# Performance work log

Measured on AMD Instinct MI355X. Metric: run time of the kernel, lower is better.

The kernel has to match this reference:

```python
import jax, jax.numpy as jnp
import numpy as np

B, T, H, I = 256, 512, 512, 256  # max batch, seq_len, hidden_size, input_size


def setup_inputs() -> dict:
    key = jax.random.key(0)
    ks = jax.random.split(key, 8)
    rnn_input_data = jax.random.normal(ks[0], (B * T, I), jnp.float32)
    # descending packed batch sizes, first one = B (enforce_sorted semantics)
    bs = jnp.sort(jax.random.randint(ks[1], (T,), B // 2, B + 1))[::-1]
    batch_sizes = bs.at[0].set(B).astype(jnp.int32)
    h0 = 0.1 * jax.random.normal(ks[2], (1, B, H), jnp.float32)
    c0 = 0.1 * jax.random.normal(ks[3], (1, B, H), jnp.float32)
    W_w = jax.random.normal(ks[4], (I, 4 * H), jnp.float32) / np.sqrt(I).astype(np.float32)
    W_b = jnp.zeros((4 * H,), jnp.float32)
    U_w = jax.random.normal(ks[5], (H, 4 * H), jnp.float32) / np.sqrt(H).astype(np.float32)
    tau = jnp.asarray(0.02, jnp.float32)
    return {"rnn_input_data": rnn_input_data, "batch_sizes": batch_sizes,
            "h0": h0, "c0": c0, "tau": tau, "W_w": W_w, "W_b": W_b, "U_w": U_w}


def reference(rnn_input_data, batch_sizes, h0, c0, tau, W_w, W_b, U_w):
    L, Bm, Hd = h0.shape
    SD = 2  # state_dim, fixed by the 2x2 A matrix
    mhu = 1.5
    A = jnp.array([[mhu, -mhu], [1.0 / mhu, 0.0]], jnp.float32)
    # faithful to source bug: data is always sliced from the front -> only first B rows used
    x0 = rnn_input_data[:Bm]  # (B, I), masked per step
    Tn = batch_sizes.shape[0]
    arangeB = jnp.arange(Bm)

    def step(carry, inp):
        h, c = carry  # (L,B,H) each
        t, bs = inp
        mask = (arangeB < bs)[:, None]  # (B,1)
        # tau-based state-space correction on first SD dims of ALL layers/rows (t != 0)
        xs = h[:, :, :SD]
        xcorr = xs + tau * jnp.einsum('lbi,ij->lbj', xs, A)
        h = h.at[:, :, :SD].set(jnp.where(t != 0, xcorr, xs))
        # single LSTMCell (num_layers == 1)
        gates = x0 @ W_w + W_b + h[0] @ U_w  # (B, 4H)
        i, f, g, o = jnp.split(gates, 4, axis=-1)
        c_new = jax.nn.sigmoid(f) * c[0] + jax.nn.sigmoid(i) * jnp.tanh(g)
        h_new = jax.nn.sigmoid(o) * jnp.tanh(c_new)
        h = h.at[0].set(jnp.where(mask, h_new, h[0]))
        c = c.at[0].set(jnp.where(mask, c_new, c[0]))
        out_t = jnp.where(mask, h[-1], 0.0)  # outputs[t, :bs] = h[-1,:bs], rest zeros
        return (h, c), out_t

    (h, c), outputs = jax.lax.scan(step, (h0, c0), (jnp.arange(Tn), batch_sizes))
    return outputs, h, c
```

## Files before the change

### kernel.cpp

```cpp
#include <hip/hip_runtime.h>


#define TN 512
#define BM 256
#define HD 512
#define ID 256

typedef __attribute__((ext_vector_type(8))) __bf16 bf16x8;
typedef __attribute__((ext_vector_type(4))) __bf16 bf16x4;
typedef __attribute__((ext_vector_type(4))) unsigned int u32x4;
typedef __attribute__((ext_vector_type(4))) float f32x4;

union ABits { u32x4 u; bf16x8 b; };
union U64x1 { bf16x4 v; unsigned long long q; };

__device__ __forceinline__ float sigm(float x) { return 1.f / (1.f + __expf(-x)); }
__device__ __forceinline__ float tanh_fast(float x) { return 1.f - 2.f / (__expf(2.f * x) + 1.f); }

__device__ __forceinline__ void store_h64(__bf16* p, unsigned long long v) {
    asm volatile("global_store_dwordx2 %0, %1, off sc0" :: "v"(p), "v"(v) : "memory");
}

__global__ void __launch_bounds__(256, 1)
lstm_persist(const float* __restrict__ x_in, const int* __restrict__ bs_in,
             const float* __restrict__ h0, const float* __restrict__ c0,
             const float* __restrict__ tau_p, const float* __restrict__ Ww,
             const float* __restrict__ Wb, const float* __restrict__ Uw,
             float* __restrict__ out, __bf16* __restrict__ hbuf,
             int* __restrict__ flags)
{
    __shared__ int   bs_lds[TN];
    __shared__ float x0_lds[16][ID + 1];
    __shared__ float hn_patch[4][16][9];
    __shared__ __align__(16) __bf16 htile[16][520];

    const int tid  = threadIdx.x;
    const int lane = tid & 63;
    const int w    = tid >> 6;
    const int bid  = blockIdx.x;

    const int xcd = bid & 7;
    const int ii  = bid >> 3;
    const int mg  = xcd * 2 + (ii >> 4);
    const int jb  = ii & 15;

    const int row0 = mg * 16;
    const int j0   = jb * 32;
    const int l15  = lane & 15;
    const int kg   = lane >> 4;
    const int gq   = lane & 3;
    const int jjq  = l15 >> 2;
    const float tau = tau_p[0];

    const int srow = 4 * w + (lane >> 4);
    const int scol = (lane & 15) * 8;

    for (int i = tid; i < TN; i += 256) bs_lds[i] = bs_in[i];
    for (int s = tid; s < 16 * (ID / 4); s += 256) {
        int r = s >> 6, cs = s & 63;
        *reinterpret_cast<float4*>(&x0_lds[r][cs * 4]) =
            reinterpret_cast<const float4*>(x_in + (size_t)(row0 + r) * ID)[cs];
    }
    __syncthreads();

    float gxv[2][4];
    {
        float a[2][4] = {};
        const int cbase = j0 + 8 * w + kg;
        for (int k = 0; k < ID; ++k) {
            float xv = x0_lds[l15][k];
            const float* wr = Ww + (size_t)k * 2048;
            #pragma unroll
            for (int g = 0; g < 4; ++g) {
                a[0][g] += xv * wr[g * HD + cbase];
                a[1][g] += xv * wr[g * HD + cbase + 4];
            }
        }
        #pragma unroll
        for (int g = 0; g < 4; ++g) {
            gxv[0][g] = a[0][g] + Wb[g * HD + cbase];
            gxv[1][g] = a[1][g] + Wb[g * HD + cbase + 4];
        }
    }

    bf16x8 ub[2][16];
    #pragma unroll
    for (int f = 0; f < 2; ++f) {
        const int ucol = gq * HD + j0 + 8 * w + 4 * f + jjq;
        #pragma unroll
        for (int ki = 0; ki < 16; ++ki) {
            const int kb = ki * 32 + kg * 8;
            bf16x8 v;
            #pragma unroll
            for (int e = 0; e < 8; ++e) v[e] = (__bf16)Uw[(size_t)(kb + e) * 2048 + ucol];
            ub[f][ki] = v;
        }
    }

    float creg[2];
    #pragma unroll
    for (int f = 0; f < 2; ++f)
        creg[f] = c0[(size_t)(row0 + l15) * HD + j0 + 8 * w + 4 * f + kg];

    const int sr = lane >> 1, ss = lane & 1;
    const int jc = j0 + 8 * w + 4 * ss;
    const bool is_store = (lane < 32);
    const bool owner = (jb == 0) && (w == 0) && (ss == 0) && is_store;
    float hprev[4] = {0.f, 0.f, 0.f, 0.f};
    float hxy0 = 0.f, hxy1 = 0.f;

    if (is_store) {
        float4 v = *reinterpret_cast<const float4*>(h0 + (size_t)(row0 + sr) * HD + jc);
        hprev[0] = v.x; hprev[1] = v.y; hprev[2] = v.z; hprev[3] = v.w;
        if (owner) { hxy0 = v.x; hxy1 = v.y; }
        U64x1 sv;
        #pragma unroll
        for (int c = 0; c < 4; ++c) sv.v[c] = (__bf16)hprev[c];
        store_h64(hbuf + (size_t)(row0 + sr) * HD + jc, sv.q);
    }
    asm volatile("s_waitcnt vmcnt(0)" ::: "memory");
    __builtin_amdgcn_sched_barrier(0);
    if (lane == 0)
        __hip_atomic_store(&flags[mg * 64 + jb * 4 + w], 1,
                           __ATOMIC_RELAXED, __HIP_MEMORY_SCOPE_AGENT);

    for (int t = 0; t < TN; ++t) {
        const __bf16* base_p = hbuf + (size_t)(t & 1) * (BM * HD);
        __bf16*       base_n = hbuf + (size_t)((t + 1) & 1) * (BM * HD);
        const int bs_t = bs_lds[t];

        if (t != 0) {
            float xs0 = hxy0, xs1 = hxy1;
            hxy0 = xs0 + tau * (1.5f * xs0 + 0.66666667f * xs1);
            hxy1 = xs1 + tau * (-1.5f * xs0);
        }

        for (int it = 0; it < (1 << 20); ++it) {
            int v = __hip_atomic_load(&flags[mg * 64 + lane],
                                      __ATOMIC_RELAXED, __HIP_MEMORY_SCOPE_AGENT);
            if (__all(v >= t + 1)) break;
            __builtin_amdgcn_s_sleep(1);
        }

        {
            const __bf16* srcp = base_p + (size_t)(row0 + srow) * HD + scol;
            u32x4 s0, s1, s2, s3;
            asm volatile(
                "global_load_dwordx4 %0, %[p], off sc0\n\t"
                "global_load_dwordx4 %1, %[p], off offset:256 sc0\n\t"
                "global_load_dwordx4 %2, %[p], off offset:512 sc0\n\t"
                "global_load_dwordx4 %3, %[p], off offset:768 sc0\n\t"
                "s_waitcnt vmcnt(0)"
                : "=&v"(s0), "=&v"(s1), "=&v"(s2), "=&v"(s3)
                : [p] "v"(srcp)
                : "memory");
            __builtin_amdgcn_sched_barrier(0);
            ABits tb;
            tb.u = s0; *reinterpret_cast<bf16x8*>(&htile[srow][scol])       = tb.b;
            tb.u = s1; *reinterpret_cast<bf16x8*>(&htile[srow][scol + 128]) = tb.b;
            tb.u = s2; *reinterpret_cast<bf16x8*>(&htile[srow][scol + 256]) = tb.b;
            tb.u = s3; *reinterpret_cast<bf16x8*>(&htile[srow][scol + 384]) = tb.b;
        }
        __syncthreads();

        bf16x8 ah[16];
        #pragma unroll
        for (int ki = 0; ki < 16; ++ki)
            ah[ki] = *reinterpret_cast<const bf16x8*>(&htile[l15][ki * 32 + kg * 8]);

        if (t != 0 && kg == 0) {
            float xs0 = (float)ah[0][0];
            float xs1 = (float)ah[0][1];
            ah[0][0] = (__bf16)(xs0 + tau * (1.5f * xs0 + 0.66666667f * xs1));
            ah[0][1] = (__bf16)(xs1 + tau * (-1.5f * xs0));
        }

        f32x4 acc0 = {0.f, 0.f, 0.f, 0.f}, acc1 = {0.f, 0.f, 0.f, 0.f};
        #pragma unroll
        for (int ki = 0; ki < 16; ++ki) {
            acc0 = __builtin_amdgcn_mfma_f32_16x16x32_bf16(ub[0][ki], ah[ki], acc0, 0, 0, 0);
            acc1 = __builtin_amdgcn_mfma_f32_16x16x32_bf16(ub[1][ki], ah[ki], acc1, 0, 0, 0);
        }

        const bool act_m = (row0 + l15) < bs_t;
        #pragma unroll
        for (int f = 0; f < 2; ++f) {
            const f32x4 a = f ? acc1 : acc0;
            float gi = a[0] + gxv[f][0];
            float gf = a[1] + gxv[f][1];
            float gg = a[2] + gxv[f][2];
            float go = a[3] + gxv[f][3];
            float cn = sigm(gf) * creg[f] + sigm(gi) * tanh_fast(gg);
            float hn = sigm(go) * tanh_fast(cn);
            if (act_m) creg[f] = cn;
            hn_patch[w][l15][4 * f + kg] = hn;
        }

        asm volatile("s_waitcnt lgkmcnt(0)" ::: "memory");
        __builtin_amdgcn_sched_barrier(0);

        if (is_store) {
            const bool act_r = (row0 + sr) < bs_t;
            float hn0 = hn_patch[w][sr][4 * ss + 0];
            float hn1 = hn_patch[w][sr][4 * ss + 1];
            float hn2 = hn_patch[w][sr][4 * ss + 2];
            float hn3 = hn_patch[w][sr][4 * ss + 3];
            float hv[4];
            hv[0] = act_r ? hn0 : hprev[0];
            hv[1] = act_r ? hn1 : hprev[1];
            hv[2] = act_r ? hn2 : hprev[2];
            hv[3] = act_r ? hn3 : hprev[3];
            if (owner) {
                if (act_r) { hxy0 = hn0; hxy1 = hn1; }
                else       { hv[0] = hxy0; hv[1] = hxy1; }
            }
            #pragma unroll
            for (int c = 0; c < 4; ++c) hprev[c] = hv[c];
            U64x1 sv;
            #pragma unroll
            for (int c = 0; c < 4; ++c) sv.v[c] = (__bf16)hv[c];
            store_h64(base_n + (size_t)(row0 + sr) * HD + jc, sv.q);
            asm volatile("s_waitcnt vmcnt(0)" ::: "memory");
            __builtin_amdgcn_sched_barrier(0);
            if (lane == 0)
                __hip_atomic_store(&flags[mg * 64 + jb * 4 + w], t + 2,
                                   __ATOMIC_RELAXED, __HIP_MEMORY_SCOPE_AGENT);
            float4 q;
            q.x = act_r ? hn0 : 0.f; q.y = act_r ? hn1 : 0.f;
            q.z = act_r ? hn2 : 0.f; q.w = act_r ? hn3 : 0.f;
            *reinterpret_cast<float4*>(out + (size_t)t * (BM * HD)
                                       + (size_t)(row0 + sr) * HD + jc) = q;
        }
    }

    if (is_store) {
        float4 p;
        p.x = hprev[0]; p.y = hprev[1]; p.z = hprev[2]; p.w = hprev[3];
        *reinterpret_cast<float4*>(out + (size_t)TN * BM * HD
                                   + (size_t)(row0 + sr) * HD + jc) = p;
    }
    {
        float* cp = out + (size_t)TN * BM * HD + (size_t)BM * HD;
        #pragma unroll
        for (int f = 0; f < 2; ++f)
            cp[(size_t)(row0 + l15) * HD + j0 + 8 * w + 4 * f + kg] = creg[f];
    }
}

extern "C" void kernel_launch(void* const* d_in, const int* in_sizes, int n_in,
                              void* d_out, int out_size, void* d_ws, size_t ws_size,
                              hipStream_t stream) {
    const float* x_in = (const float*)d_in[0];
    const int*   bs   = (const int*)d_in[1];
    const float* h0   = (const float*)d_in[2];
    const float* c0   = (const float*)d_in[3];
    const float* tau  = (const float*)d_in[4];
    const float* Ww   = (const float*)d_in[5];
    const float* Wb   = (const float*)d_in[6];
    const float* Uw   = (const float*)d_in[7];
    float* out = (float*)d_out;

    int*    flags = (int*)d_ws;
    __bf16* hbuf  = (__bf16*)((char*)d_ws + 4096);

    (void)hipMemsetAsync(d_ws, 0, 4096, stream);

    hipLaunchKernelGGL(lstm_persist, dim3(256), dim3(256), 0, stream,
                       x_in, bs, h0, c0, tau, Ww, Wb, Uw, out, hbuf, flags);
}
```

Measured before the change: 2.366 ms.

## Load h operands straight into registers, drop LDS staging and skip inactive row groups

Each wave now loads its own 16 rows of the previous hidden state directly from global memory into MFMA operand registers. This removes the LDS tile, the block-wide __syncthreads, and the LDS round-trip used to transpose the gate outputs, which are now redistributed with cross-lane shuffles. Row groups entirely beyond the current batch size skip the wait, the GEMM and the flag update and only write zeros. The trade-off is four times more global load traffic per wave (redundant across waves) and a skip path that relies on descending batch sizes so consumers never wait on the skipped flags.

After: 3.682 ms. 55.6% more time.

```diff
diff --git a/kernel.cpp b/kernel.cpp
--- a/kernel.cpp
+++ b/kernel.cpp
@@ -31,8 +31,6 @@
 {
     __shared__ int   bs_lds[TN];
     __shared__ float x0_lds[16][ID + 1];
-    __shared__ float hn_patch[4][16][9];
-    __shared__ __align__(16) __bf16 htile[16][520];
 
     const int tid  = threadIdx.x;
     const int lane = tid & 63;
@@ -52,9 +50,6 @@
     const int jjq  = l15 >> 2;
     const float tau = tau_p[0];
 
-    const int srow = 4 * w + (lane >> 4);
-    const int scol = (lane & 15) * 8;
-
     for (int i = tid; i < TN; i += 256) bs_lds[i] = bs_in[i];
     for (int s = tid; s < 16 * (ID / 4); s += 256) {
         int r = s >> 6, cs = s & 63;
@@ -102,8 +97,9 @@
     for (int f = 0; f < 2; ++f)
         creg[f] = c0[(size_t)(row0 + l15) * HD + j0 + 8 * w + 4 * f + kg];
 
-    const int sr = lane >> 1, ss = lane & 1;
-    const int jc = j0 + 8 * w + 4 * ss;
+    const int sr   = lane >> 1, ss = lane & 1;
+    const int sr16 = (lane >> 1) & 15;
+    const int jc   = j0 + 8 * w + 4 * ss;
     const bool is_store = (lane < 32);
     const bool owner = (jb == 0) && (w == 0) && (ss == 0) && is_store;
     float hprev[4] = {0.f, 0.f, 0.f, 0.f};
@@ -135,6 +131,15 @@
             hxy1 = xs1 + tau * (-1.5f * xs0);
         }
 
+        if (row0 >= bs_t) {
+            if (is_store) {
+                float4 z = {0.f, 0.f, 0.f, 0.f};
+                *reinterpret_cast<float4*>(out + (size_t)t * (BM * HD)
+                                           + (size_t)(row0 + sr) * HD + jc) = z;
+            }
+            continue;
+        }
+
         for (int it = 0; it < (1 << 20); ++it) {
             int v = __hip_atomic_load(&flags[mg * 64 + lane],
                                       __ATOMIC_RELAXED, __HIP_MEMORY_SCOPE_AGENT);
@@ -142,31 +147,46 @@
             __builtin_amdgcn_s_sleep(1);
         }
 
+        const __bf16* arow = base_p + (size_t)(row0 + l15) * HD + kg * 8;
+        u32x4 r0,r1,r2,r3,r4,r5,r6,r7,r8,r9,r10,r11,r12,r13,r14,r15;
+        asm volatile(
+            "global_load_dwordx4 %0, %[p], off sc0\n\t"
+            "global_load_dwordx4 %1, %[p], off offset:64 sc0\n\t"
+            "global_load_dwordx4 %2, %[p], off offset:128 sc0\n\t"
+            "global_load_dwordx4 %3, %[p], off offset:192 sc0\n\t"
+            "global_load_dwordx4 %4, %[p], off offset:256 sc0\n\t"
+            "global_load_dwordx4 %5, %[p], off offset:320 sc0\n\t"
+            "global_load_dwordx4 %6, %[p], off offset:384 sc0\n\t"
+            "global_load_dwordx4 %7, %[p], off offset:448 sc0\n\t"
+            "global_load_dwordx4 %8, %[p], off offset:512 sc0\n\t"
+            "global_load_dwordx4 %9, %[p], off offset:576 sc0\n\t"
+            "global_load_dwordx4 %10, %[p], off offset:640 sc0\n\t"
+            "global_load_dwordx4 %11, %[p], off offset:704 sc0\n\t"
+            "global_load_dwordx4 %12, %[p], off offset:768 sc0\n\t"
+            "global_load_dwordx4 %13, %[p], off offset:832 sc0\n\t"
+            "global_load_dwordx4 %14, %[p], off offset:896 sc0\n\t"
+            "global_load_dwordx4 %15, %[p], off offset:960 sc0\n\t"
+            "s_waitcnt vmcnt(0)"
+            : "=&v"(r0), "=&v"(r1), "=&v"(r2), "=&v"(r3),
+              "=&v"(r4), "=&v"(r5), "=&v"(r6), "=&v"(r7),
+              "=&v"(r8), "=&v"(r9), "=&v"(r10), "=&v"(r11),
+              "=&v"(r12), "=&v"(r13), "=&v"(r14), "=&v"(r15)
+            : [p] "v"(arow)
+            : "memory");
+        __builtin_amdgcn_sched_barrier(0);
+
+        bf16x8 ah[16];
         {
-            const __bf16* srcp = base_p + (size_t)(row0 + srow) * HD + scol;
-            u32x4 s0, s1, s2, s3;
-            asm volatile(
-                "global_load_dwordx4 %0, %[p], off sc0\n\t"
-                "global_load_dwordx4 %1, %[p], off offset:256 sc0\n\t"
-                "global_load_dwordx4 %2, %[p], off offset:512 sc0\n\t"
-                "global_load_dwordx4 %3, %[p], off offset:768 sc0\n\t"
-                "s_waitcnt vmcnt(0)"
-                : "=&v"(s0), "=&v"(s1), "=&v"(s2), "=&v"(s3)
-                : [p] "v"(srcp)
-                : "memory");
-            __builtin_amdgcn_sched_barrier(0);
             ABits tb;
-            tb.u = s0; *reinterpret_cast<bf16x8*>(&htile[srow][scol])       = tb.b;
-            tb.u = s1; *reinterpret_cast<bf16x8*>(&htile[srow][scol + 128]) = tb.b;
-            tb.u = s2; *reinterpret_cast<bf16x8*>(&htile[srow][scol + 256]) = tb.b;
-            tb.u = s3; *reinterpret_cast<bf16x8*>(&htile[srow][scol + 384]) = tb.b;
-        }
-        __syncthreads();
-
-        bf16x8 ah[16];
-        #pragma unroll
-        for (int ki = 0; ki < 16; ++ki)
-            ah[ki] = *reinterpret_cast<const bf16x8*>(&htile[l15][ki * 32 + kg * 8]);
+            tb.u = r0;  ah[0]  = tb.b;  tb.u = r1;  ah[1]  = tb.b;
+            tb.u = r2;  ah[2]  = tb.b;  tb.u = r3;  ah[3]  = tb.b;
+            tb.u = r4;  ah[4]  = tb.b;  tb.u = r5;  ah[5]  = tb.b;
+            tb.u = r6;  ah[6]  = tb.b;  tb.u = r7;  ah[7]  = tb.b;
+            tb.u = r8;  ah[8]  = tb.b;  tb.u = r9;  ah[9]  = tb.b;
+            tb.u = r10; ah[10] = tb.b;  tb.u = r11; ah[11] = tb.b;
+            tb.u = r12; ah[12] = tb.b;  tb.u = r13; ah[13] = tb.b;
+            tb.u = r14; ah[14] = tb.b;  tb.u = r15; ah[15] = tb.b;
+        }
 
         if (t != 0 && kg == 0) {
             float xs0 = (float)ah[0][0];
@@ -183,35 +203,43 @@
         }
 
         const bool act_m = (row0 + l15) < bs_t;
-        #pragma unroll
-        for (int f = 0; f < 2; ++f) {
-            const f32x4 a = f ? acc1 : acc0;
-            float gi = a[0] + gxv[f][0];
-            float gf = a[1] + gxv[f][1];
-            float gg = a[2] + gxv[f][2];
-            float go = a[3] + gxv[f][3];
-            float cn = sigm(gf) * creg[f] + sigm(gi) * tanh_fast(gg);
-            float hn = sigm(go) * tanh_fast(cn);
-            if (act_m) creg[f] = cn;
-            hn_patch[w][l15][4 * f + kg] = hn;
-        }
-
-        asm volatile("s_waitcnt lgkmcnt(0)" ::: "memory");
-        __builtin_amdgcn_sched_barrier(0);
+        float hnf0, hnf1;
+        {
+            float gi = acc0[0] + gxv[0][0];
+            float gf = acc0[1] + gxv[0][1];
+            float gg = acc0[2] + gxv[0][2];
+            float go = acc0[3] + gxv[0][3];
+            float cn = sigm(gf) * creg[0] + sigm(gi) * tanh_fast(gg);
+            hnf0 = sigm(go) * tanh_fast(cn);
+            if (act_m) creg[0] = cn;
+        }
+        {
+            float gi = acc1[0] + gxv[1][0];
+            float gf = acc1[1] + gxv[1][1];
+            float gg = acc1[2] + gxv[1][2];
+            float go = acc1[3] + gxv[1][3];
+            float cn = sigm(gf) * creg[1] + sigm(gi) * tanh_fast(gg);
+            hnf1 = sigm(go) * tanh_fast(cn);
+            if (act_m) creg[1] = cn;
+        }
+
+        float av[4], bv[4];
+        #pragma unroll
+        for (int c = 0; c < 4; ++c) {
+            av[c] = __shfl(hnf0, 16 * c + sr16);
+            bv[c] = __shfl(hnf1, 16 * c + sr16);
+        }
 
         if (is_store) {
             const bool act_r = (row0 + sr) < bs_t;
-            float hn0 = hn_patch[w][sr][4 * ss + 0];
-            float hn1 = hn_patch[w][sr][4 * ss + 1];
-            float hn2 = hn_patch[w][sr][4 * ss + 2];
-            float hn3 = hn_patch[w][sr][4 * ss + 3];
+            float hn[4];
+            #pragma unroll
+            for (int c = 0; c < 4; ++c) hn[c] = ss ? bv[c] : av[c];
             float hv[4];
-            hv[0] = act_r ? hn0 : hprev[0];
-            hv[1] = act_r ? hn1 : hprev[1];
-            hv[2] = act_r ? hn2 : hprev[2];
-            hv[3] = act_r ? hn3 : hprev[3];
+            #pragma unroll
+            for (int c = 0; c < 4; ++c) hv[c] = act_r ? hn[c] : hprev[c];
             if (owner) {
-                if (act_r) { hxy0 = hn0; hxy1 = hn1; }
+                if (act_r) { hxy0 = hn[0]; hxy1 = hn[1]; }
                 else       { hv[0] = hxy0; hv[1] = hxy1; }
             }
             #pragma unroll
@@ -225,14 +253,16 @@
             if (lane == 0)
                 __hip_atomic_store(&flags[mg * 64 + jb * 4 + w], t + 2,
                                    __ATOMIC_RELAXED, __HIP_MEMORY_SCOPE_AGENT);
+
             float4 q;
-            q.x = act_r ? hn0 : 0.f; q.y = act_r ? hn1 : 0.f;
-            q.z = act_r ? hn2 : 0.f; q.w = act_r ? hn3 : 0.f;
+            q.x = act_r ? hn[0] : 0.f; q.y = act_r ? hn[1] : 0.f;
+            q.z = act_r ? hn[2] : 0.f; q.w = act_r ? hn[3] : 0.f;
             *reinterpret_cast<float4*>(out + (size_t)t * (BM * HD)
                                        + (size_t)(row0 + sr) * HD + jc) = q;
         }
     }
 
+    if (owner) { hprev[0] = hxy0; hprev[1] = hxy1; }
     if (is_store) {
         float4 p;
         p.x = hprev[0]; p.y = hprev[1]; p.z = hprev[2]; p.w = hprev[3];
```
